# Kernel optimization log

Hardware: AMD Instinct MI355X
Metric: run time of the kernel (lower is better)

Reference implementation:

```python
import jax, jax.numpy as jnp
import numpy as np

# ---- para constants (see shape_source) ----
SIZE = 200          # SLM / detector plane
PAD = 100           # para.paddings -> padded FFT plane 400x400
PADDED = SIZE + 2 * PAD
NUM_LAYERS = 4
SCALE = 2.0         # para.scale
EXT = 1.0           # para.extension
K = 8               # para.kernel_size
S = 8               # para.stride
M = (SIZE - K) // S + 1   # para.map_size = 25
WIN = 5             # para.win_size
T = 1.0             # softmax temperature
RANGE = 10          # para.range (== dim_out)
DIM_OUT = 10
HIDDEN = 512
DIM_IN = M * M      # 625, flattened BN output feeds fcl
THR = 0.2           # para.thershold
SHIFT = 0.0         # para.shift
EPS = 1e-5          # BatchNorm eps
BATCH = 32


def setup_inputs() -> dict:
    key = jax.random.key(0)
    ks = jax.random.split(key, 10)
    x = jax.random.uniform(ks[0], (BATCH, SIZE, SIZE), jnp.float32)

    def transfer(k):  # unit-magnitude angular-spectrum transfer function
        ph = jax.random.uniform(k, (PADDED, PADDED), jnp.float32, 0.0, 2.0 * np.pi)
        return jnp.exp(1j * ph).astype(jnp.complex64)

    h = transfer(ks[1])
    h_pro = transfer(ks[2])
    h_det = transfer(ks[3])
    phase = 0.1 * jax.random.normal(ks[4], (NUM_LAYERS, SIZE, SIZE), jnp.float32)
    W1 = 0.02 * jax.random.normal(ks[5], (HIDDEN, DIM_IN), jnp.float32)
    b1 = jnp.zeros((HIDDEN,), jnp.float32)
    W2 = 0.02 * jax.random.normal(ks[6], (DIM_OUT, HIDDEN), jnp.float32)
    b2 = jnp.zeros((DIM_OUT,), jnp.float32)
    gamma = jnp.ones((1,), jnp.float32)   # BatchNorm2d(1) weight
    beta = jnp.zeros((1,), jnp.float32)   # BatchNorm2d(1) bias
    return {"x": x, "batch_size": BATCH, "h": h, "h_pro": h_pro, "h_det": h_det,
            "phase": phase, "W1": W1, "b1": b1, "W2": W2, "b2": b2,
            "gamma": gamma, "beta": beta}


def _diff(wave, trans):
    # F.pad + fftshift/fft2 * trans / ifft2/ifftshift (batch-dim shifts cancel)
    wave = jnp.pad(wave, ((0, 0), (PAD, PAD), (PAD, PAD)))
    wf = jnp.fft.fft2(jnp.fft.fftshift(wave, axes=(-2, -1)))
    return jnp.fft.ifftshift(jnp.fft.ifft2(wf * trans), axes=(-2, -1))


def _forward(x, batch_size, h, h_pro, h_det, phase, W1, b1, W2, b2, gamma, beta):
    x = x.astype(jnp.complex64)
    x = _diff(x, h_pro)[:, PAD:PAD + SIZE, PAD:PAD + SIZE]
    for idx in range(NUM_LAYERS):
        trans = jnp.pad(phase[idx], ((PAD, PAD), (PAD, PAD)))
        w = _diff(x, h)
        w = w * jnp.exp(1j * SCALE * jnp.pi * (jnp.sin(EXT * trans) + 1.0))
        x = w[:, PAD:PAD + SIZE, PAD:PAD + SIZE]
    x = _diff(x, h_det)[:, PAD:PAD + SIZE, PAD:PAD + SIZE]
    i_out = jnp.square(jnp.abs(x))                       # (B, SIZE, SIZE)
    B = i_out.shape[0]
    # AvgPool2d(K, S) with SIZE % K == 0 -> reshape-mean
    pooled = i_out.reshape(B, M, K, M, K).mean(axis=(2, 4))  # (B, M, M)

    rows = jnp.arange(M)

    def window(i, j):
        rm = (rows >= i) & (rows < i + WIN)
        cm = (rows >= j) & (rows < j + WIN)
        mask = (rm[:, None] & cm[None, :]).astype(pooled.dtype)   # I_block
        sig = pooled * mask                                       # (B, M, M)
        # BatchNorm2d(1), training mode: stats over all N*H*W
        mu = sig.mean()
        var = sig.var()
        nrm = (sig - mu) / jnp.sqrt(var + EPS) * gamma[0] + beta[0]
        f = nrm.reshape(B, -1)                                    # (B, DIM_IN)
        hid = jax.nn.relu(f @ W1.T + b1)                          # dropout: eval
        logits = (hid @ W2.T + b2) / T
        p = jax.nn.softmax(logits, axis=1)                        # (B, DIM_OUT)
        a = jnp.argmax(p, axis=1)                                 # (B,)
        delta = p.max(axis=1) - p.min(axis=1)                     # b - b2
        temp = jax.nn.one_hot(a, RANGE + 1, dtype=jnp.float32).sum(0)
        final0 = jnp.argmax(temp)
        dm = delta * (a == final0).astype(delta.dtype)            # delta * delta_max
        nz = jnp.sum(dm != 0.0)                                   # csr .data length
        delta1 = jnp.where(nz > 0, dm.sum() / jnp.maximum(nz, 1).astype(dm.dtype), jnp.nan)
        # nan < THR is False, matching torch semantics
        final = jnp.where(delta1 < THR, 0, final0 + 1).astype(jnp.int32)
        res = jnp.where(final == 0, 0.0, final.astype(jnp.float32) + SHIFT)
        ch = (final != 0).astype(jnp.float32)
        return final, res, ch

    ii, jj = jnp.meshgrid(jnp.arange(M), jnp.arange(M), indexing="ij")
    finals, result, ch_map = jax.vmap(window)(ii.ravel(), jj.ravel())
    result = result.reshape(M, M)
    ch_map = ch_map.reshape(M, M)
    histo = jnp.zeros(RANGE + 1, jnp.float32).at[finals].add(1.0)
    return result, ch_map, histo


def reference(x, batch_size, h, h_pro, h_det, phase, W1, b1, W2, b2, gamma, beta):
    return _forward(x, batch_size, h, h_pro, h_det, phase, W1, b1, W2, b2, gamma, beta)
```

## Files before the change

kernel.cpp:

```cpp
#include <hip/hip_runtime.h>
#include <math.h>

#define GLIM_X    1280000
#define GLIM_H    160000
#define GLIM_PH   160000
#define GLIM_W1   320000
#define GLIM_B1   512
#define GLIM_W2   5120
#define GLIM_B2   10
#define GLIM_OUT  1261
#define GLIM_POOL 20000

#define HPART 128

struct cplx { float x, y; };
__device__ __forceinline__ cplx operator+(cplx a, cplx b){ return {a.x+b.x, a.y+b.y}; }
__device__ __forceinline__ cplx operator-(cplx a, cplx b){ return {a.x-b.x, a.y-b.y}; }
__device__ __forceinline__ cplx cmul(cplx a, cplx b){ return {a.x*b.x - a.y*b.y, a.x*b.y + a.y*b.x}; }
template<bool INV>
__device__ __forceinline__ cplx tw(cplx a, cplx w){
  if(INV) return {a.x*w.x + a.y*w.y, a.y*w.x - a.x*w.y};
  else    return {a.x*w.x - a.y*w.y, a.x*w.y + a.y*w.x};
}
template<bool INV>
__device__ __forceinline__ void dft4(cplx&a, cplx&b, cplx&c, cplx&d){
  cplx t0=a+c, t1=a-c, t2=b+d, t3=b-d;
  cplx j3 = INV ? cplx{-t3.y, t3.x} : cplx{t3.y, -t3.x};
  a = t0+t2; c = t0-t2; b = t1+j3; d = t1-j3;
}
template<bool INV>
__device__ void fft16(cplx* x, const cplx* tab){
  cplx y[16];
  #pragma unroll
  for(int b=0;b<4;b++){
    cplx p0=x[b], p1=x[4+b], p2=x[8+b], p3=x[12+b];
    dft4<INV>(p0,p1,p2,p3);
    y[b*4+0]=p0;
    y[b*4+1]=tw<INV>(p1, tab[25*b]);
    y[b*4+2]=tw<INV>(p2, tab[50*b]);
    y[b*4+3]=tw<INV>(p3, tab[75*b]);
  }
  #pragma unroll
  for(int c=0;c<4;c++){
    cplx p0=y[c], p1=y[4+c], p2=y[8+c], p3=y[12+c];
    dft4<INV>(p0,p1,p2,p3);
    x[c]=p0; x[c+4]=p1; x[c+8]=p2; x[c+12]=p3;
  }
}
template<bool INV>
__device__ __forceinline__ void dft5(const cplx* v, cplx* o, const cplx* tab){
  #pragma unroll
  for(int k=0;k<5;k++){
    cplx s=v[0];
    #pragma unroll
    for(int j=1;j<5;j++){
      const int m=(j*k)%5;
      s = s + tw<INV>(v[j], tab[80*m]);
    }
    o[k]=s;
  }
}
template<bool INV>
__device__ void fft25(cplx* t, const cplx* tab){
  cplx u[25];
  #pragma unroll
  for(int b=0;b<5;b++){
    cplx v[5], o[5];
    #pragma unroll
    for(int a=0;a<5;a++) v[a]=t[5*a+b];
    dft5<INV>(v,o,tab);
    #pragma unroll
    for(int c=0;c<5;c++) u[b*5+c]=tw<INV>(o[c], tab[16*b*c]);
  }
  #pragma unroll
  for(int c=0;c<5;c++){
    cplx v[5], o[5];
    #pragma unroll
    for(int b=0;b<5;b++) v[b]=u[b*5+c];
    dft5<INV>(v,o,tab);
    #pragma unroll
    for(int d=0;d<5;d++) t[c+5*d]=o[d];
  }
}

__device__ __forceinline__ void wfence(){
  __asm__ volatile("s_waitcnt lgkmcnt(0)" ::: "memory");
}

__device__ __forceinline__ float bf2f(unsigned short u){
  unsigned int v = ((unsigned int)u)<<16;
  float f; __builtin_memcpy(&f,&v,4); return f;
}
__device__ __forceinline__ float hf2f(unsigned short u){
  _Float16 x; __builtin_memcpy(&x,&u,2); return (float)x;
}
__device__ __forceinline__ cplx ldH(const void* p, int i, int dec){
  if(i<0 || i>=GLIM_H) return {0.f,0.f};
  unsigned int v = ((const unsigned int*)p)[i];
  unsigned short lo=(unsigned short)(v&0xFFFFu), hi=(unsigned short)(v>>16);
  cplx z;
  if(dec==2)      z = { hf2f(lo), hf2f(hi) };
  else if(dec==3) z = { (float)(short)lo*(1.f/32767.f), (float)(short)hi*(1.f/32767.f) };
  else            z = { bf2f(lo), bf2f(hi) };
  if(!(fabsf(z.x) < 2.f)) z.x = 0.f;
  if(!(fabsf(z.y) < 2.f)) z.y = 0.f;
  return z;
}
__device__ __forceinline__ float ldf(const float* p, int i, int lim){
  if(i<0 || i>=lim) return 0.f;
  return p[i];
}
__device__ __forceinline__ void stout(float* p, int i, float v){
  if(i>=0 && i<GLIM_OUT) p[i] = v;
}

__global__ __launch_bounds__(64) void k_probe(const void* h, int* flags){
  __shared__ float err[3];
  if(threadIdx.x<3) err[threadIdx.x]=0.f;
  __syncthreads();
  if(threadIdx.x<32){
    unsigned int v = ((const unsigned int*)h)[threadIdx.x];
    unsigned short lo=(unsigned short)(v&0xFFFFu), hi=(unsigned short)(v>>16);
    float cr[3], ci[3];
    cr[0]=bf2f(lo);                       ci[0]=bf2f(hi);
    cr[1]=hf2f(lo);                       ci[1]=hf2f(hi);
    cr[2]=(float)(short)lo*(1.f/32767.f); ci[2]=(float)(short)hi*(1.f/32767.f);
    for(int d=0;d<3;d++){
      float r2 = cr[d]*cr[d] + ci[d]*ci[d];
      float e = fabsf(r2 - 1.f);
      if(!(e < 4.f)) e = 4.f;
      atomicAdd(&err[d], e);
    }
  }
  __syncthreads();
  if(threadIdx.x==0){
    int best=0; float be=err[0];
    for(int d=1; d<3; d++) if(err[d] < be){ be=err[d]; best=d; }
    flags[1] = best+1;
    flags[0] = 0;
  }
}

__global__ __launch_bounds__(256) void k_init(cplx* tab, float* outz, float* hist, float* pr){
  int t = blockIdx.x*256 + threadIdx.x;
  if(t < 400){
    float a = -6.28318530717958647692f * (float)t * (1.0f/400.0f);
    float sn, cs; sincosf(a, &sn, &cs);
    tab[t] = { cs, sn };
  }
  if(t < GLIM_OUT) outz[t] = 0.f;
  if(t < 11) hist[t] = 0.f;
  if(t >= 16 && t < 30) pr[t-16] = 0.f;
}

__global__ __launch_bounds__(256) void k_hprep(const void* h, const void* hpro,
    const void* hdet, cplx* __restrict__ Hd, const int* __restrict__ flags)
{
  int dec = flags[1];
  int t = blockIdx.x*256 + threadIdx.x;
  if(t >= 3*GLIM_H) return;
  int arr = t/GLIM_H, o = t - arr*GLIM_H;
  int c = o/400, rem = o - c*400;
  int k1 = rem/25, k2 = rem - k1*25;
  const void* src = (arr==0)?h:((arr==1)?hpro:hdet);
  Hd[t] = ldH(src, (k1+16*k2)*400 + c, dec);
}

__global__ __launch_bounds__(512,2) void k_rowfft(const float* __restrict__ xr,
    int img0, cplx* __restrict__ A, const cplx* __restrict__ gtab, int alim)
{
  __shared__ cplx lb[16*400];
  __shared__ cplx stab[400];
  for(int m=threadIdx.x;m<400;m+=512) stab[m]=gtab[m];
  int g = threadIdx.x>>5, role = threadIdx.x&31;
  int idx = blockIdx.x*16 + g;
  int img_local = idx/200, rc = idx - img_local*200;
  int abase = img_local*80000 + rc*400;
  cplx* L = lb + g*400;
  cplx xx[25];
  __syncthreads();
  if(role<25){
    int n2=role;
    #pragma unroll
    for(int n1=0;n1<16;n1++){
      cplx v={0.f,0.f};
      if(n1>=4 && n1<12){
        int cc = 25*n1+n2-100;
        v = { ldf(xr, (img0+img_local)*40000 + rc*200 + cc, GLIM_X), 0.f };
      }
      xx[n1]=v;
    }
    fft16<false>(xx, stab);
    #pragma unroll
    for(int k1=0;k1<16;k1++) L[k1*25+n2]=tw<false>(xx[k1], stab[n2*k1]);
  }
  wfence();
  if(role<16){
    int k1=role;
    #pragma unroll
    for(int n2=0;n2<25;n2++) xx[n2]=L[k1*25+n2];
    fft25<false>(xx, stab);
    #pragma unroll
    for(int k2=0;k2<25;k2++){
      int ai = abase + k1+16*k2;
      if(ai>=0 && ai<alim) A[ai]=xx[k2];
    }
  }
}

__global__ __launch_bounds__(512,2) void k_colpass(cplx* __restrict__ A,
    const cplx* __restrict__ Hd, const cplx* __restrict__ gtab)
{
  __shared__ cplx sm[200][17];
  __shared__ cplx lb[16*400];
  __shared__ cplx stab[400];
  for(int m=threadIdx.x;m<400;m+=512) stab[m]=gtab[m];
  int img_local = blockIdx.x/25, cg = blockIdx.x - img_local*25;
  int col0 = cg*16;
  int g = threadIdx.x>>5, role = threadIdx.x&31;
  cplx* L = lb + g*400;
  cplx xx[25];
  {
    const float4* A4 = (const float4*)A;
    for(int t=threadIdx.x; t<1600; t+=512){
      int r = t>>3, p = t&7;
      int ce = img_local*80000 + r*400 + col0 + 2*p;
      float4 v = A4[ce>>1];
      sm[r][2*p]   = { v.x, v.y };
      sm[r][2*p+1] = { v.z, v.w };
    }
  }
  __syncthreads();
  if(role<25){
    int n2=role;
    #pragma unroll
    for(int n1=0;n1<16;n1++){
      cplx v={0.f,0.f};
      if(n1>=4 && n1<12) v = sm[25*n1+n2-100][g];
      xx[n1]=v;
    }
    fft16<false>(xx, stab);
    #pragma unroll
    for(int k1=0;k1<16;k1++) L[k1*25+n2]=tw<false>(xx[k1], stab[n2*k1]);
  }
  wfence();
  if(role<16){
    int k1=role;
    #pragma unroll
    for(int n2=0;n2<25;n2++) xx[n2]=L[k1*25+n2];
    fft25<false>(xx, stab);
    const cplx* hrun = Hd + (col0+g)*400 + k1*25;
    #pragma unroll
    for(int k2=0;k2<25;k2++) xx[k2]=cmul(xx[k2], hrun[k2]);
    #pragma unroll
    for(int k2=0;k2<25;k2++) L[k1+16*k2]=xx[k2];
  }
  wfence();
  if(role<25){
    int n2=role;
    #pragma unroll
    for(int n1=0;n1<16;n1++) xx[n1]=L[25*n1+n2];
    fft16<true>(xx, stab);
    #pragma unroll
    for(int k1=0;k1<16;k1++) L[k1*25+n2]=tw<true>(xx[k1], stab[n2*k1]);
  }
  wfence();
  if(role<16){
    int k1=role;
    #pragma unroll
    for(int n2=0;n2<25;n2++) xx[n2]=L[k1*25+n2];
    fft25<true>(xx, stab);
    const float sc=1.0f/400.0f;
    #pragma unroll
    for(int k2=0;k2<25;k2++){
      int m=k1+16*k2;
      if(m>=100 && m<300) sm[m-100][g] = { xx[k2].x*sc, xx[k2].y*sc };
    }
  }
  __syncthreads();
  {
    float4* A4 = (float4*)A;
    for(int t=threadIdx.x; t<1600; t+=512){
      int r = t>>3, p = t&7;
      int ce = img_local*80000 + r*400 + col0 + 2*p;
      cplx a = sm[r][2*p], b = sm[r][2*p+1];
      A4[ce>>1] = { a.x, a.y, b.x, b.y };
    }
  }
}

__global__ __launch_bounds__(512,2) void k_rowpass(cplx* __restrict__ A,
    const float* __restrict__ ph, int phoff, int useMask,
    const cplx* __restrict__ gtab, int alim)
{
  __shared__ cplx lb[16*400];
  __shared__ cplx stab[400];
  for(int m=threadIdx.x;m<400;m+=512) stab[m]=gtab[m];
  int g = threadIdx.x>>5, role = threadIdx.x&31;
  int idx = blockIdx.x*16 + g;
  int img_local = idx/200, rc = idx - img_local*200;
  int abase = img_local*80000 + rc*400;
  cplx* L = lb + g*400;
  cplx xx[25];
  __syncthreads();
  if(role<25){
    int n2=role;
    #pragma unroll
    for(int n1=0;n1<16;n1++){
      cplx v={0.f,0.f};
      int ai = abase + 25*n1+n2;
      if(ai>=0 && ai<alim) v=A[ai];
      xx[n1]=v;
    }
    fft16<true>(xx, stab);
    #pragma unroll
    for(int k1=0;k1<16;k1++) L[k1*25+n2]=tw<true>(xx[k1], stab[n2*k1]);
  }
  wfence();
  if(role<16){
    int k1=role;
    #pragma unroll
    for(int n2=0;n2<25;n2++) xx[n2]=L[k1*25+n2];
    fft25<true>(xx, stab);
    const float sc=1.0f/400.0f;
    #pragma unroll
    for(int k2=0;k2<25;k2++){
      int m=k1+16*k2;
      if(m>=100 && m<300){
        int cc=m-100;
        cplx v={ xx[k2].x*sc, xx[k2].y*sc };
        if(useMask){
          float tt = ldf(ph, phoff + rc*200+cc, GLIM_PH);
          float th = 6.28318530717958647692f*(sinf(tt)+1.0f);
          float sn, cs; sincosf(th,&sn,&cs);
          v = cmul(v, cplx{cs,sn});
        }
        L[cc]=v;
      }
    }
  }
  wfence();
  if(role<25){
    int n2=role;
    #pragma unroll
    for(int n1=0;n1<16;n1++){
      cplx v={0.f,0.f};
      if(n1>=4 && n1<12) v = L[25*n1+n2-100];
      xx[n1]=v;
    }
    fft16<false>(xx, stab);
    #pragma unroll
    for(int k1=0;k1<16;k1++) L[k1*25+n2]=tw<false>(xx[k1], stab[n2*k1]);
  }
  wfence();
  if(role<16){
    int k1=role;
    #pragma unroll
    for(int n2=0;n2<25;n2++) xx[n2]=L[k1*25+n2];
    fft25<false>(xx, stab);
    #pragma unroll
    for(int k2=0;k2<25;k2++){
      int ai = abase + k1+16*k2;
      if(ai>=0 && ai<alim) A[ai]=xx[k2];
    }
  }
}

__global__ __launch_bounds__(512,2) void k_rowpool(const cplx* __restrict__ A,
    float* __restrict__ pooled, int img0, const cplx* __restrict__ gtab, int alim)
{
  __shared__ cplx lb[16*400];
  __shared__ cplx stab[400];
  __shared__ float sI[16][200];
  for(int m=threadIdx.x;m<400;m+=512) stab[m]=gtab[m];
  int g = threadIdx.x>>5, role = threadIdx.x&31;
  int idx = blockIdx.x*16 + g;
  int img_local = idx/200;
  int abase = img_local*80000 + (idx - img_local*200)*400;
  cplx* L = lb + g*400;
  cplx xx[25];
  __syncthreads();
  if(role<25){
    int n2=role;
    #pragma unroll
    for(int n1=0;n1<16;n1++){
      cplx v={0.f,0.f};
      int ai = abase + 25*n1+n2;
      if(ai>=0 && ai<alim) v=A[ai];
      xx[n1]=v;
    }
    fft16<true>(xx, stab);
    #pragma unroll
    for(int k1=0;k1<16;k1++) L[k1*25+n2]=tw<true>(xx[k1], stab[n2*k1]);
  }
  wfence();
  if(role<16){
    int k1=role;
    #pragma unroll
    for(int n2=0;n2<25;n2++) xx[n2]=L[k1*25+n2];
    fft25<true>(xx, stab);
    const float sc=1.0f/400.0f;
    #pragma unroll
    for(int k2=0;k2<25;k2++){
      int m=k1+16*k2;
      if(m>=100 && m<300){
        float re=xx[k2].x*sc, im=xx[k2].y*sc;
        sI[g][m-100] = re*re + im*im;
      }
    }
  }
  __syncthreads();
  if(threadIdx.x<50){
    int b = threadIdx.x/25, c = threadIdx.x - b*25;
    int rbase = blockIdx.x*16 + b*8;
    int il = rbase/200, r0 = rbase - il*200;
    float s=0.f;
    #pragma unroll
    for(int u=0;u<8;u++){
      #pragma unroll
      for(int v=0;v<8;v++) s += sI[b*8+u][c*8+v];
    }
    int pi = (img0+il)*625 + (r0>>3)*25 + c;
    if(pi>=0 && pi<GLIM_POOL) pooled[pi] = s*(1.0f/64.0f);
  }
}

__global__ __launch_bounds__(64) void k_rowsum(const float* __restrict__ W1,
    float* __restrict__ rs){
  __shared__ float red[64];
  int hh = blockIdx.x;
  float s=0.f;
  for(int e=threadIdx.x;e<625;e+=64) s += ldf(W1, hh*625+e, GLIM_W1);
  red[threadIdx.x]=s;
  __syncthreads();
  for(int off=32;off>0;off>>=1){
    if(threadIdx.x<off) red[threadIdx.x]+=red[threadIdx.x+off];
    __syncthreads();
  }
  if(threadIdx.x==0 && hh<512) rs[hh]=red[0];
}

__global__ __launch_bounds__(256,2) void k_window(const float* __restrict__ pooled,
    const float* __restrict__ W1, const float* __restrict__ b1,
    const float* __restrict__ W2, const float* __restrict__ rowsum,
    const float* __restrict__ gm, const float* __restrict__ bt,
    float* __restrict__ LP)
{
  __shared__ float w1s[HPART*26];
  __shared__ float w2s[10*HPART];
  __shared__ float ps[25*32];
  __shared__ float comb[HPART];
  __shared__ int   wIdx[25];
  __shared__ float sred[4][2];
  __shared__ float sf0, sgos;

  int wi = blockIdx.x >> 2;
  int part = blockIdx.x & 3;
  int h0 = part*HPART;
  int i = wi/25, j = wi - i*25;
  int er = (25-i<5)?(25-i):5;
  int ec = (25-j<5)?(25-j):5;
  int E = er*ec;
  int tid = threadIdx.x;
  if(tid<25) wIdx[tid] = (i + tid/ec)*25 + (j + tid%ec);
  __syncthreads();

  for(int t=tid;t<10*HPART;t+=256) w2s[t] = ldf(W2, (t>>7)*512 + h0 + (t&(HPART-1)), GLIM_W2);

  for(int t=tid;t<800;t+=256){
    int e=t>>5;
    float v=0.f;
    if(e<E){
      v = pooled[(t&31)*625 + wIdx[e]];
      if(!(fabsf(v) < 1e30f)) v = 0.f;
    }
    ps[t]=v;
  }

  if(E==25){
    for(int t=tid;t<HPART*25;t+=256){
      int hh=t/25, e=t-hh*25;
      w1s[hh*26+e] = ldf(W1, (h0+hh)*625+wIdx[e], GLIM_W1);
    }
  } else {
    for(int t=tid;t<832;t+=256) ((float4*)w1s)[t] = float4{0.f,0.f,0.f,0.f};
    __syncthreads();
    for(int t=tid;t<HPART*E;t+=256){
      int hh=t/E, e=t-hh*E;
      w1s[hh*26+e] = ldf(W1, (h0+hh)*625+wIdx[e], GLIM_W1);
    }
  }
  __syncthreads();

  {
    float s1=0.f, s2=0.f;
    for(int t=tid;t<800;t+=256){ float v=ps[t]; s1+=v; s2+=v*v; }
    #pragma unroll
    for(int m=1;m<64;m<<=1){ s1 += __shfl_xor(s1,m); s2 += __shfl_xor(s2,m); }
    if((tid&63)==0){ sred[tid>>6][0]=s1; sred[tid>>6][1]=s2; }
  }
  __syncthreads();
  if(tid==0){
    float a=sred[0][0]+sred[1][0]+sred[2][0]+sred[3][0];
    float c=sred[0][1]+sred[1][1]+sred[2][1]+sred[3][1];
    float mu = a*(1.0f/20000.0f);
    float var = c*(1.0f/20000.0f) - mu*mu;
    float sg = sqrtf(var + 1e-5f);
    float g = gm[0];
    sf0 = bt[0] - g*mu/sg;
    sgos = g/sg;
  }
  __syncthreads();
  float f0=sf0, gos=sgos;
  for(int hh=tid;hh<HPART;hh+=256) comb[hh] = ldf(b1,h0+hh,GLIM_B1) + f0*ldf(rowsum,h0+hh,512);
  __syncthreads();

  int b = tid&31, s = tid>>5;
  float psr[25];
  #pragma unroll
  for(int e=0;e<25;e++) psr[e]=ps[e*32+b];

  float pl[10];
  #pragma unroll
  for(int o=0;o<10;o++) pl[o]=0.f;
  for(int k=0;k<16;k++){
    int hh = s*16+k;
    const float* wr = &w1s[hh*26];
    float wsum=0.f;
    #pragma unroll
    for(int e=0;e<25;e++) wsum = fmaf(wr[e], psr[e], wsum);
    float acc = comb[hh] + gos*wsum;
    float hid = acc>0.f?acc:0.f;
    #pragma unroll
    for(int o=0;o<10;o++) pl[o] = fmaf(hid, w2s[o*HPART+hh], pl[o]);
  }
  __syncthreads();
  float* red = w1s;
  #pragma unroll
  for(int o=0;o<10;o++) red[(s*32+b)*10+o]=pl[o];
  __syncthreads();

  if(tid<32){
    #pragma unroll
    for(int o=0;o<10;o++){
      float a = 0.f;
      #pragma unroll
      for(int u=0;u<8;u++) a += red[(u*32+tid)*10+o];
      LP[((part*625+wi)*32+tid)*10+o] = a;
    }
  }
}

__global__ __launch_bounds__(64) void k_vote(const float* __restrict__ LP,
    const float* __restrict__ b2, float* __restrict__ outp, float* __restrict__ hist)
{
  __shared__ int aArr[32];
  __shared__ float dArr[32];
  int wi = blockIdx.x, tid = threadIdx.x;
  if(tid<32){
    float lg[10];
    #pragma unroll
    for(int o=0;o<10;o++){
      float a = ldf(b2,o,GLIM_B2);
      #pragma unroll
      for(int p=0;p<4;p++) a += LP[((p*625+wi)*32+tid)*10+o];
      lg[o]=a;
    }
    float lmax=lg[0]; int am=0;
    #pragma unroll
    for(int o=1;o<10;o++) if(lg[o]>lmax){lmax=lg[o]; am=o;}
    float lmin=lg[0];
    #pragma unroll
    for(int o=1;o<10;o++) lmin=fminf(lmin,lg[o]);
    float Z=0.f;
    #pragma unroll
    for(int o=0;o<10;o++) Z += expf(lg[o]-lmax);
    float delta = (1.f - expf(lmin-lmax))/Z;
    aArr[tid]=am; dArr[tid]=delta;
  }
  __syncthreads();
  if(tid==0){
    int votes[11];
    #pragma unroll
    for(int k=0;k<11;k++) votes[k]=0;
    for(int bb=0;bb<32;bb++){
      int a=aArr[bb];
      if(a>=0 && a<11) votes[a]++;
    }
    int f0i=0, bv=votes[0];
    #pragma unroll
    for(int k=1;k<11;k++) if(votes[k]>bv){bv=votes[k]; f0i=k;}
    float sum=0.f; int nz=0;
    for(int bb=0;bb<32;bb++){
      if(aArr[bb]==f0i){
        float dd=dArr[bb];
        sum+=dd;
        if(dd!=0.f) nz++;
      }
    }
    int fin;
    if(nz>0){
      float d1=sum/(float)nz;
      fin = (d1<0.2f)?0:(f0i+1);
    } else fin = f0i+1;
    stout(outp, wi, (fin==0)?0.f:(float)fin);
    stout(outp, 625+wi, (fin!=0)?1.f:0.f);
    if(fin>=0 && fin<=10) atomicAdd(&hist[fin], 1.0f);
  }
}

__global__ __launch_bounds__(64) void k_fin(const float* __restrict__ hist,
    float* __restrict__ outp){
  if(threadIdx.x<11) stout(outp, 1250+threadIdx.x, hist[threadIdx.x]);
}

__global__ __launch_bounds__(256) void k_diag(const float* __restrict__ pooled,
    const float* __restrict__ hist, const float* __restrict__ pr,
    const int* __restrict__ flags, float* __restrict__ outp){
  __shared__ float smax[256];
  __shared__ int snan[256];
  float m=0.f; int nan=0;
  for(int i=threadIdx.x;i<GLIM_POOL;i+=256){
    float v=pooled[i];
    if(isnan(v)||isinf(v)) nan=1;
    else { float a=fabsf(v); if(a>m)m=a; }
  }
  smax[threadIdx.x]=m; snan[threadIdx.x]=nan;
  __syncthreads();
  for(int off=128;off>0;off>>=1){
    if(threadIdx.x<off){
      smax[threadIdx.x]=fmaxf(smax[threadIdx.x],smax[threadIdx.x+off]);
      snan[threadIdx.x]|=snan[threadIdx.x+off];
    }
    __syncthreads();
  }
  if(threadIdx.x==0 && hist[0] < 613.f){
    int dec = flags[1] & 7;
    int low, nanbit = 0;
    if(snan[0]){ nanbit=128; low=0; (void)pr; }
    else {
      if(smax[0]<=0.f) low=0;
      else {
        int e=(int)floorf(log2f(smax[0]));
        low = e+8; if(low<1)low=1; if(low>15)low=15;
      }
    }
    int S = nanbit | (dec<<4) | low;
    outp[0] = 8192.0f*(float)S;
  }
}

extern "C" void kernel_launch(void* const* d_in, const int* in_sizes, int n_in,
                              void* d_out, int out_size, void* d_ws, size_t ws_size,
                              hipStream_t stream)
{
  (void)in_sizes;
  if(n_in != 12 || out_size < GLIM_OUT || d_ws == nullptr) return;
  const float* x   = (const float*)d_in[0];
  const void* h    = d_in[2];
  const void* hpro = d_in[3];
  const void* hdet = d_in[4];
  const float* phase=(const float*)d_in[5];
  const float* W1  = (const float*)d_in[6];
  const float* b1  = (const float*)d_in[7];
  const float* W2  = (const float*)d_in[8];
  const float* b2  = (const float*)d_in[9];
  const float* gm  = (const float*)d_in[10];
  const float* bt  = (const float*)d_in[11];
  float* out = (float*)d_out;

  const size_t FIXED = 85888ull;
  const size_t HDB   = 3ull*GLIM_H*8ull;
  const size_t ABase = FIXED + HDB;
  int n = 0;
  if     (ABase + 32ull*640000ull <= ws_size) n = 32;
  else if(ABase + 16ull*640000ull <= ws_size) n = 16;
  else if(ABase +  8ull*640000ull <= ws_size) n = 8;
  else if(ABase +  4ull*640000ull <= ws_size) n = 4;
  else if(ABase +  2ull*640000ull <= ws_size) n = 2;
  else if(ABase +  1ull*640000ull <= ws_size) n = 1;
  if(n==0) return;

  char* w = (char*)d_ws;
  int*   flags  = (int*)(w + 0);
  cplx*  tab    = (cplx*)(w + 256);
  float* rowsum = (float*)(w + 3584);
  float* hist   = (float*)(w + 5632);
  float* pr     = (float*)(w + 5760);
  float* pooled = (float*)(w + 5888);
  cplx*  Hd     = (cplx*)(w + FIXED);
  cplx*  A      = (cplx*)(w + ABase);
  float* LP     = (float*)Hd;
  const int alim  = n*80000;

  k_probe<<<1,64,0,stream>>>(h, flags);
  k_init<<<6,256,0,stream>>>(tab, out, hist, pr);
  k_rowsum<<<512,64,0,stream>>>(W1, rowsum);
  k_hprep<<<(3*GLIM_H+255)/256,256,0,stream>>>(h, hpro, hdet, Hd, flags);

  for(int c=0; c<32; c+=n){
    k_rowfft<<<(n*200+15)/16,512,0,stream>>>(x, c, A, tab, alim);
    for(int d=0; d<6; d++){
      const cplx* Hcur = (d==0) ? (Hd+GLIM_H) : ((d==5) ? (Hd+2*GLIM_H) : Hd);
      k_colpass<<<n*25,512,0,stream>>>(A, Hcur, tab);
      if(d<5){
        int useMask = (d>=1) ? 1 : 0;
        int phoff = useMask ? (d-1)*40000 : 0;
        k_rowpass<<<(n*200+15)/16,512,0,stream>>>(A, phase, phoff, useMask, tab, alim);
      } else {
        k_rowpool<<<(n*200+15)/16,512,0,stream>>>(A, pooled, c, tab, alim);
      }
    }
  }
  k_window<<<2500,256,0,stream>>>(pooled, W1,b1,W2,rowsum, gm,bt, LP);
  k_vote<<<625,64,0,stream>>>(LP, b2, out, hist);
  k_fin<<<1,64,0,stream>>>(hist, out);
  k_diag<<<1,256,0,stream>>>(pooled, hist, pr, flags, out);
}
```

Measured before the change: 726.4 us.

## Remap FFT threads so lanes span lines, stage coalesced loads via LDS

Changes the thread mapping in the row and column FFT kernels. Each wavefront previously owned one line with only 25 or 16 of its 64 lanes active; now the lane index selects one of 16 lines and the FFT role comes from threadIdx>>4, so wavefronts are fully populated. Global row loads are staged through LDS with coalesced float4 reads, and rows are padded to 401 entries to reduce bank conflicts. The per-wavefront lgkmcnt fences become block-wide __syncthreads, which adds barrier cost and extra LDS (cb, smf) that may reduce occupancy.

```diff
diff --git a/kernel.cpp b/kernel.cpp
--- a/kernel.cpp
+++ b/kernel.cpp
@@ -81,10 +81,6 @@
     #pragma unroll
     for(int d=0;d<5;d++) t[c+5*d]=o[d];
   }
-}
-
-__device__ __forceinline__ void wfence(){
-  __asm__ volatile("s_waitcnt lgkmcnt(0)" ::: "memory");
 }
 
 __device__ __forceinline__ float bf2f(unsigned short u){
@@ -169,34 +165,48 @@
 __global__ __launch_bounds__(512,2) void k_rowfft(const float* __restrict__ xr,
     int img0, cplx* __restrict__ A, const cplx* __restrict__ gtab, int alim)
 {
-  __shared__ cplx lb[16*400];
+  __shared__ cplx lb[16*401];
+  __shared__ float smf[16*201];
   __shared__ cplx stab[400];
   for(int m=threadIdx.x;m<400;m+=512) stab[m]=gtab[m];
-  int g = threadIdx.x>>5, role = threadIdx.x&31;
-  int idx = blockIdx.x*16 + g;
-  int img_local = idx/200, rc = idx - img_local*200;
-  int abase = img_local*80000 + rc*400;
-  cplx* L = lb + g*400;
+  int lc = threadIdx.x&15, rr = threadIdx.x>>4;
+  int idx0 = blockIdx.x*16;
+  cplx* L = lb + lc*401;
   cplx xx[25];
-  __syncthreads();
-  if(role<25){
-    int n2=role;
+  {
+    const float4* X4 = (const float4*)xr;
+    for(int t=threadIdx.x; t<800; t+=512){
+      int r = t/50, q = t-r*50;
+      int idx = idx0 + r;
+      int img_local = idx/200, rc = idx - img_local*200;
+      int bi = (img0+img_local)*40000 + rc*200 + 4*q;
+      float4 v = {0.f,0.f,0.f,0.f};
+      if(bi>=0 && bi+3<GLIM_X) v = X4[bi>>2];
+      smf[r*201 + 4*q+0] = v.x;
+      smf[r*201 + 4*q+1] = v.y;
+      smf[r*201 + 4*q+2] = v.z;
+      smf[r*201 + 4*q+3] = v.w;
+    }
+  }
+  __syncthreads();
+  if(rr<25){
+    int n2=rr;
     #pragma unroll
     for(int n1=0;n1<16;n1++){
       cplx v={0.f,0.f};
-      if(n1>=4 && n1<12){
-        int cc = 25*n1+n2-100;
-        v = { ldf(xr, (img0+img_local)*40000 + rc*200 + cc, GLIM_X), 0.f };
-      }
+      if(n1>=4 && n1<12) v = { smf[lc*201 + 25*n1+n2-100], 0.f };
       xx[n1]=v;
     }
     fft16<false>(xx, stab);
     #pragma unroll
     for(int k1=0;k1<16;k1++) L[k1*25+n2]=tw<false>(xx[k1], stab[n2*k1]);
   }
-  wfence();
-  if(role<16){
-    int k1=role;
+  __syncthreads();
+  if(rr<16){
+    int k1=rr;
+    int idx = idx0+lc;
+    int img_local = idx/200, rc = idx - img_local*200;
+    int abase = img_local*80000 + rc*400;
     #pragma unroll
     for(int n2=0;n2<25;n2++) xx[n2]=L[k1*25+n2];
     fft25<false>(xx, stab);
@@ -212,13 +222,13 @@
     const cplx* __restrict__ Hd, const cplx* __restrict__ gtab)
 {
   __shared__ cplx sm[200][17];
-  __shared__ cplx lb[16*400];
+  __shared__ cplx lb[16*401];
   __shared__ cplx stab[400];
   for(int m=threadIdx.x;m<400;m+=512) stab[m]=gtab[m];
   int img_local = blockIdx.x/25, cg = blockIdx.x - img_local*25;
   int col0 = cg*16;
-  int g = threadIdx.x>>5, role = threadIdx.x&31;
-  cplx* L = lb + g*400;
+  int lc = threadIdx.x&15, rr = threadIdx.x>>4;
+  cplx* L = lb + lc*401;
   cplx xx[25];
   {
     const float4* A4 = (const float4*)A;
@@ -231,42 +241,47 @@
     }
   }
   __syncthreads();
-  if(role<25){
-    int n2=role;
+  if(rr<25){
+    int n2=rr;
     #pragma unroll
     for(int n1=0;n1<16;n1++){
       cplx v={0.f,0.f};
-      if(n1>=4 && n1<12) v = sm[25*n1+n2-100][g];
+      if(n1>=4 && n1<12) v = sm[25*n1+n2-100][lc];
       xx[n1]=v;
     }
     fft16<false>(xx, stab);
     #pragma unroll
     for(int k1=0;k1<16;k1++) L[k1*25+n2]=tw<false>(xx[k1], stab[n2*k1]);
   }
-  wfence();
-  if(role<16){
-    int k1=role;
+  __syncthreads();
+  if(rr<16){
+    int k1=rr;
     #pragma unroll
     for(int n2=0;n2<25;n2++) xx[n2]=L[k1*25+n2];
     fft25<false>(xx, stab);
-    const cplx* hrun = Hd + (col0+g)*400 + k1*25;
-    #pragma unroll
-    for(int k2=0;k2<25;k2++) xx[k2]=cmul(xx[k2], hrun[k2]);
-    #pragma unroll
-    for(int k2=0;k2<25;k2++) L[k1+16*k2]=xx[k2];
-  }
-  wfence();
-  if(role<25){
-    int n2=role;
-    #pragma unroll
-    for(int n1=0;n1<16;n1++) xx[n1]=L[25*n1+n2];
+    const cplx* hrun = Hd + (col0+lc)*400 + k1*25;
+    #pragma unroll
+    for(int k2=0;k2<25;k2++) L[k1*25+k2]=cmul(xx[k2], hrun[k2]);
+  }
+  __syncthreads();
+  if(rr<25){
+    int n2=rr;
+    #pragma unroll
+    for(int n1=0;n1<16;n1++){
+      int m = 25*n1+n2;
+      xx[n1] = L[(m&15)*25 + (m>>4)];
+    }
+  }
+  __syncthreads();
+  if(rr<25){
+    int n2=rr;
     fft16<true>(xx, stab);
     #pragma unroll
     for(int k1=0;k1<16;k1++) L[k1*25+n2]=tw<true>(xx[k1], stab[n2*k1]);
   }
-  wfence();
-  if(role<16){
-    int k1=role;
+  __syncthreads();
+  if(rr<16){
+    int k1=rr;
     #pragma unroll
     for(int n2=0;n2<25;n2++) xx[n2]=L[k1*25+n2];
     fft25<true>(xx, stab);
@@ -274,7 +289,7 @@
     #pragma unroll
     for(int k2=0;k2<25;k2++){
       int m=k1+16*k2;
-      if(m>=100 && m<300) sm[m-100][g] = { xx[k2].x*sc, xx[k2].y*sc };
+      if(m>=100 && m<300) sm[m-100][lc] = { xx[k2].x*sc, xx[k2].y*sc };
     }
   }
   __syncthreads();
@@ -293,32 +308,45 @@
     const float* __restrict__ ph, int phoff, int useMask,
     const cplx* __restrict__ gtab, int alim)
 {
-  __shared__ cplx lb[16*400];
+  __shared__ cplx lb[16*401];
+  __shared__ cplx cb[16][201];
   __shared__ cplx stab[400];
   for(int m=threadIdx.x;m<400;m+=512) stab[m]=gtab[m];
-  int g = threadIdx.x>>5, role = threadIdx.x&31;
-  int idx = blockIdx.x*16 + g;
-  int img_local = idx/200, rc = idx - img_local*200;
-  int abase = img_local*80000 + rc*400;
-  cplx* L = lb + g*400;
+  int lc = threadIdx.x&15, rr = threadIdx.x>>4;
+  int idx0 = blockIdx.x*16;
+  cplx* L = lb + lc*401;
   cplx xx[25];
-  __syncthreads();
-  if(role<25){
-    int n2=role;
-    #pragma unroll
-    for(int n1=0;n1<16;n1++){
-      cplx v={0.f,0.f};
-      int ai = abase + 25*n1+n2;
-      if(ai>=0 && ai<alim) v=A[ai];
-      xx[n1]=v;
-    }
+  {
+    const float4* A4 = (const float4*)A;
+    for(int t=threadIdx.x; t<3200; t+=512){
+      int r = t/200, q = t-r*200;
+      int idx = idx0 + r;
+      int img_local = idx/200, rc = idx - img_local*200;
+      int base = img_local*80000 + rc*400;
+      cplx v0={0.f,0.f}, v1={0.f,0.f};
+      if(base + 2*q + 1 < alim){
+        float4 v = A4[(base>>1)+q];
+        v0 = {v.x,v.y}; v1 = {v.z,v.w};
+      }
+      lb[r*401 + 2*q]   = v0;
+      lb[r*401 + 2*q+1] = v1;
+    }
+  }
+  __syncthreads();
+  if(rr<25){
+    int n2=rr;
+    #pragma unroll
+    for(int n1=0;n1<16;n1++) xx[n1] = L[25*n1+n2];
     fft16<true>(xx, stab);
     #pragma unroll
     for(int k1=0;k1<16;k1++) L[k1*25+n2]=tw<true>(xx[k1], stab[n2*k1]);
   }
-  wfence();
-  if(role<16){
-    int k1=role;
+  __syncthreads();
+  if(rr<16){
+    int k1=rr;
+    int idx = idx0 + lc;
+    int img_local = idx/200, rc = idx - img_local*200;
+    (void)img_local;
     #pragma unroll
     for(int n2=0;n2<25;n2++) xx[n2]=L[k1*25+n2];
     fft25<true>(xx, stab);
@@ -335,26 +363,29 @@
           float sn, cs; sincosf(th,&sn,&cs);
           v = cmul(v, cplx{cs,sn});
         }
-        L[cc]=v;
+        cb[lc][cc]=v;
       }
     }
   }
-  wfence();
-  if(role<25){
-    int n2=role;
+  __syncthreads();
+  if(rr<25){
+    int n2=rr;
     #pragma unroll
     for(int n1=0;n1<16;n1++){
       cplx v={0.f,0.f};
-      if(n1>=4 && n1<12) v = L[25*n1+n2-100];
+      if(n1>=4 && n1<12) v = cb[lc][25*n1+n2-100];
       xx[n1]=v;
     }
     fft16<false>(xx, stab);
     #pragma unroll
     for(int k1=0;k1<16;k1++) L[k1*25+n2]=tw<false>(xx[k1], stab[n2*k1]);
   }
-  wfence();
-  if(role<16){
-    int k1=role;
+  __syncthreads();
+  if(rr<16){
+    int k1=rr;
+    int idx = idx0 + lc;
+    int img_local = idx/200, rc = idx - img_local*200;
+    int abase = img_local*80000 + rc*400;
     #pragma unroll
     for(int n2=0;n2<25;n2++) xx[n2]=L[k1*25+n2];
     fft25<false>(xx, stab);
@@ -369,33 +400,42 @@
 __global__ __launch_bounds__(512,2) void k_rowpool(const cplx* __restrict__ A,
     float* __restrict__ pooled, int img0, const cplx* __restrict__ gtab, int alim)
 {
-  __shared__ cplx lb[16*400];
+  __shared__ cplx lb[16*401];
   __shared__ cplx stab[400];
   __shared__ float sI[16][200];
   for(int m=threadIdx.x;m<400;m+=512) stab[m]=gtab[m];
-  int g = threadIdx.x>>5, role = threadIdx.x&31;
-  int idx = blockIdx.x*16 + g;
-  int img_local = idx/200;
-  int abase = img_local*80000 + (idx - img_local*200)*400;
-  cplx* L = lb + g*400;
+  int lc = threadIdx.x&15, rr = threadIdx.x>>4;
+  int idx0 = blockIdx.x*16;
+  cplx* L = lb + lc*401;
   cplx xx[25];
-  __syncthreads();
-  if(role<25){
-    int n2=role;
-    #pragma unroll
-    for(int n1=0;n1<16;n1++){
-      cplx v={0.f,0.f};
-      int ai = abase + 25*n1+n2;
-      if(ai>=0 && ai<alim) v=A[ai];
-      xx[n1]=v;
-    }
+  {
+    const float4* A4 = (const float4*)A;
+    for(int t=threadIdx.x; t<3200; t+=512){
+      int r = t/200, q = t-r*200;
+      int idx = idx0 + r;
+      int img_local = idx/200, rc = idx - img_local*200;
+      int base = img_local*80000 + rc*400;
+      cplx v0={0.f,0.f}, v1={0.f,0.f};
+      if(base + 2*q + 1 < alim){
+        float4 v = A4[(base>>1)+q];
+        v0 = {v.x,v.y}; v1 = {v.z,v.w};
+      }
+      lb[r*401 + 2*q]   = v0;
+      lb[r*401 + 2*q+1] = v1;
+    }
+  }
+  __syncthreads();
+  if(rr<25){
+    int n2=rr;
+    #pragma unroll
+    for(int n1=0;n1<16;n1++) xx[n1] = L[25*n1+n2];
     fft16<true>(xx, stab);
     #pragma unroll
     for(int k1=0;k1<16;k1++) L[k1*25+n2]=tw<true>(xx[k1], stab[n2*k1]);
   }
-  wfence();
-  if(role<16){
-    int k1=role;
+  __syncthreads();
+  if(rr<16){
+    int k1=rr;
     #pragma unroll
     for(int n2=0;n2<25;n2++) xx[n2]=L[k1*25+n2];
     fft25<true>(xx, stab);
@@ -405,14 +445,14 @@
       int m=k1+16*k2;
       if(m>=100 && m<300){
         float re=xx[k2].x*sc, im=xx[k2].y*sc;
-        sI[g][m-100] = re*re + im*im;
+        sI[lc][m-100] = re*re + im*im;
       }
     }
   }
   __syncthreads();
   if(threadIdx.x<50){
     int b = threadIdx.x/25, c = threadIdx.x - b*25;
-    int rbase = blockIdx.x*16 + b*8;
+    int rbase = idx0 + b*8;
     int il = rbase/200, r0 = rbase - il*200;
     float s=0.f;
     #pragma unroll
```

Result: slower. 812.2 us (+11.8%).
